# Kernel optimization log

Hardware: AMD Instinct MI355X
Metric: run time of the kernel (lower is better)

Reference implementation:

```python
import jax, jax.numpy as jnp
import numpy as np

H = 256  # hidden_dim
N = 500000  # num_orbitals
M = 8192  # num_molecules


def setup_inputs() -> dict:
    key = jax.random.key(0)
    ks = jax.random.split(key, 12)
    s = lambda fan_in: 1.0 / np.sqrt(fan_in)
    inp = {
        "orbital_embeddings": jax.random.normal(ks[0], (N, H), dtype=jnp.float32),
        "batch": jnp.sort(jax.random.randint(ks[1], (N,), 0, M, dtype=jnp.int32)),
        "num_molecules": M,
        # attention MLP: Linear(H, H//2) -> ReLU -> Linear(H//2, 1)
        "aW1": jax.random.uniform(ks[2], (H, H // 2), jnp.float32, -s(H), s(H)),
        "ab1": jnp.zeros((H // 2,), jnp.float32),
        "aW2": jax.random.uniform(ks[3], (H // 2, 1), jnp.float32, -s(H // 2), s(H // 2)),
        "ab2": jnp.zeros((1,), jnp.float32),
        # global head: Linear(H,H)->ReLU->Linear(H,H//2)->ReLU->Linear(H//2,1)
        "gW1": jax.random.uniform(ks[4], (H, H), jnp.float32, -s(H), s(H)),
        "gb1": jnp.zeros((H,), jnp.float32),
        "gW2": jax.random.uniform(ks[5], (H, H // 2), jnp.float32, -s(H), s(H)),
        "gb2": jnp.zeros((H // 2,), jnp.float32),
        "gW3": jax.random.uniform(ks[6], (H // 2, 1), jnp.float32, -s(H // 2), s(H // 2)),
        "gb3": jnp.zeros((1,), jnp.float32),
    }
    return inp


def reference(orbital_embeddings, batch, num_molecules, aW1, ab1, aW2, ab2,
              gW1, gb1, gW2, gb2, gW3, gb3):
    # attention logits: [N, 1] (dropout is identity in eval mode)
    h = jax.nn.relu(orbital_embeddings @ aW1 + ab1)
    logits = h @ aW2 + ab2  # [N, 1]

    # per-molecule (segment) softmax over orbitals, numerically stable
    lg = logits[:, 0]  # [N]
    seg_max = jax.ops.segment_max(lg, batch, num_segments=num_molecules)  # [M]
    seg_max = jnp.where(jnp.isfinite(seg_max), seg_max, 0.0)  # empty segments
    ex = jnp.exp(lg - seg_max[batch])  # [N]
    denom = jax.ops.segment_sum(ex, batch, num_segments=num_molecules)  # [M]
    w = ex / denom[batch]  # [N]

    # weighted scatter-add pooling -> [M, H]
    weighted = orbital_embeddings * w[:, None]
    mol = jax.ops.segment_sum(weighted, batch, num_segments=num_molecules)

    # global head MLP -> [M, 1]
    g = jax.nn.relu(mol @ gW1 + gb1)
    g = jax.nn.relu(g @ gW2 + gb2)
    return g @ gW3 + gb3
```

## Files before the change

kernel.cpp:

```cpp
#include <hip/hip_runtime.h>
#include <hip/hip_bf16.h>

#define H      256
#define CAP    64
#define GRID12 1024
#define MMAX   16

typedef _Float16 f16x8 __attribute__((ext_vector_type(8)));
typedef float    f32x4 __attribute__((ext_vector_type(4)));

__global__ __launch_bounds__(256) void k0_pack(
    const float* __restrict__ aW1, const float* __restrict__ gW1,
    const float* __restrict__ gW2,
    _Float16* __restrict__ aW1F, float* __restrict__ gW1P, float* __restrict__ gW2P)
{
    int idx = blockIdx.x * 256 + threadIdx.x;
    int stride = gridDim.x * 256;
    for (int e8 = idx; e8 < 4096; e8 += stride) {
        int l = e8 & 63, kknt = e8 >> 6;
        int kk = kknt & 7, nt = kknt >> 3;
        int j = nt*16 + (l & 15);
        int kbase = kk*32 + (l >> 4)*8;
        f16x8 v;
        #pragma unroll
        for (int e = 0; e < 8; ++e) v[e] = (_Float16)aW1[(kbase + e)*128 + j];
        *reinterpret_cast<f16x8*>(aW1F + e8*8) = v;
    }
    for (int e = idx; e < 64*256*4; e += stride) {
        int s = e & 3, j = (e >> 2) & 255, kq = e >> 10;
        gW1P[e] = gW1[(kq*4+s)*256 + j];
    }
    for (int e = idx; e < 64*128*4; e += stride) {
        int s = e & 3, j = (e >> 2) & 127, kq = e >> 9;
        gW2P[e] = gW2[(kq*4+s)*128 + j];
    }
}

__global__ __launch_bounds__(256) void k2a_starts(
    const int* __restrict__ batch, int* __restrict__ starts, int N, int M)
{
    int i = blockIdx.x * 256 + threadIdx.x;
    if (i >= N) return;
    int b = batch[i];
    if (i == 0) {
        for (int m = 0; m <= b; ++m) starts[m] = 0;
    } else {
        int p = batch[i-1];
        for (int m = p + 1; m <= b; ++m) starts[m] = i;
    }
    if (i == N - 1) {
        for (int m = b + 1; m <= M; ++m) starts[m] = N;
    }
}

__global__ __launch_bounds__(256) void k12_fused(
    const float* __restrict__ emb, const int* __restrict__ starts,
    const _Float16* __restrict__ aW1F, const float* __restrict__ ab1,
    const float* __restrict__ aW2, const float* __restrict__ ab2,
    float* __restrict__ mol, int M)
{
    __shared__ __align__(16) _Float16 eh[CAP * H];
    __shared__ float pr[4][CAP];
    __shared__ float wl[CAP];
    __shared__ int   sst[2*MMAX];

    const int t = threadIdx.x, w = t >> 6, l = t & 63;
    const int bid = blockIdx.x;
    char* ldsb = reinterpret_cast<char*>(eh);
    const f32x4 zero = {0.f, 0.f, 0.f, 0.f};

    if (t < 2*MMAX) {
        int idx = bid + (t >> 1)*GRID12 + (t & 1);
        sst[t] = starts[idx <= M ? idx : M];
    }

    f16x8 bf[2][8];
    #pragma unroll
    for (int nt2 = 0; nt2 < 2; ++nt2)
        #pragma unroll
        for (int kk = 0; kk < 8; ++kk)
            bf[nt2][kk] = *reinterpret_cast<const f16x8*>(
                aW1F + (size_t)(((2*w + nt2)*8 + kk)*64 + l)*8);

    float b1v[2], w2v[2];
    #pragma unroll
    for (int nt2 = 0; nt2 < 2; ++nt2) {
        int j = 32*w + nt2*16 + (l & 15);
        b1v[nt2] = ab1[j];
        w2v[nt2] = aW2[j];
    }
    const float bo = ab2[0];

    __syncthreads();

    int k = 0, start = 0, end = 0;
    for (;;) {
        if (k >= MMAX || bid + (size_t)k*GRID12 >= (size_t)M) return;
        start = sst[2*k]; end = sst[2*k+1];
        if (start < end) break;
        mol[(size_t)(bid + k*GRID12)*H + t] = 0.f;
        ++k;
    }

    int c0 = start;
    int cc = min(CAP, end - c0);
    float4 pv[16];

#define ISSUE(C0, CC) do {                                                      \
    _Pragma("unroll")                                                           \
    for (int j = 0; j < 8; ++j) {                                               \
        int ci = t + j*256;                                                     \
        int r = ci >> 5, c8 = ci & 31;                                          \
        int rr = r < (CC) ? r : (CC) - 1;                                       \
        const float4* pp = reinterpret_cast<const float4*>(                     \
            emb + (size_t)((C0) + rr)*H) + c8*2;                                \
        pv[2*j] = pp[0]; pv[2*j+1] = pp[1];                                     \
    } } while (0)

    ISSUE(c0, cc);
    float mx = -INFINITY, s = 0.f, acc = 0.f;

    for (;;) {
        const int  cur_m  = bid + k*GRID12;
        const int  cur_cc = cc;
        const bool last_chunk = (c0 + CAP >= end);

        __syncthreads();

        #pragma unroll
        for (int j = 0; j < 8; ++j) {
            int ci = t + j*256;
            int r = ci >> 5, c8 = ci & 31;
            float4 v0 = pv[2*j], v1 = pv[2*j+1];
            f16x8 hv;
            hv[0]=(_Float16)v0.x; hv[1]=(_Float16)v0.y; hv[2]=(_Float16)v0.z; hv[3]=(_Float16)v0.w;
            hv[4]=(_Float16)v1.x; hv[5]=(_Float16)v1.y; hv[6]=(_Float16)v1.z; hv[7]=(_Float16)v1.w;
            int wb = (r*512 + c8*16) ^ ((r & 7) << 4);
            *reinterpret_cast<f16x8*>(ldsb + wb) = hv;
        }

        int nk = k, nc0 = c0 + CAP, nend = end;
        bool have_next = true;
        if (last_chunk) {
            ++nk;
            for (;;) {
                if (nk >= MMAX || bid + (size_t)nk*GRID12 >= (size_t)M) { have_next = false; break; }
                int ns = sst[2*nk], ne = sst[2*nk+1];
                if (ns < ne) { nc0 = ns; nend = ne; break; }
                mol[(size_t)(bid + nk*GRID12)*H + t] = 0.f;
                ++nk;
            }
        }
        int ncc = 0;
        if (have_next) { ncc = min(CAP, nend - nc0); ISSUE(nc0, ncc); }
        __syncthreads();

        #pragma unroll
        for (int rt = 0; rt < 4; ++rt) {
            int row   = rt*16 + (l & 15);
            int rbase = row*512 + (l >> 4)*16;
            int swz   = (row & 7) << 4;
            f32x4 a20 = zero, a21 = zero;
            #pragma unroll
            for (int kk = 0; kk < 8; ++kk) {
                f16x8 af = *reinterpret_cast<const f16x8*>(ldsb + ((rbase + kk*64) ^ swz));
                a20 = __builtin_amdgcn_mfma_f32_16x16x32_f16(af, bf[0][kk], a20, 0, 0, 0);
                a21 = __builtin_amdgcn_mfma_f32_16x16x32_f16(af, bf[1][kk], a21, 0, 0, 0);
            }
            #pragma unroll
            for (int r = 0; r < 4; ++r) {
                float h0 = a20[r] + b1v[0]; h0 = h0 > 0.f ? h0 : 0.f;
                float h1 = a21[r] + b1v[1]; h1 = h1 > 0.f ? h1 : 0.f;
                float p = h0*w2v[0] + h1*w2v[1];
                p += __shfl_xor(p, 1, 64);
                p += __shfl_xor(p, 2, 64);
                p += __shfl_xor(p, 4, 64);
                p += __shfl_xor(p, 8, 64);
                if ((l & 15) == 0) pr[w][rt*16 + (l >> 4)*4 + r] = p;
            }
        }
        __syncthreads();

        float lg = -INFINITY;
        if (l < cur_cc) lg = pr[0][l] + pr[1][l] + pr[2][l] + pr[3][l] + bo;
        float mc = lg;
        mc = fmaxf(mc, __shfl_xor(mc, 1, 64));
        mc = fmaxf(mc, __shfl_xor(mc, 2, 64));
        mc = fmaxf(mc, __shfl_xor(mc, 4, 64));
        mc = fmaxf(mc, __shfl_xor(mc, 8, 64));
        mc = fmaxf(mc, __shfl_xor(mc, 16, 64));
        mc = fmaxf(mc, __shfl_xor(mc, 32, 64));
        float mxn = fmaxf(mx, mc);
        float rsc = __expf(mx - mxn);
        float e = (l < cur_cc) ? __expf(lg - mxn) : 0.f;
        float sc = e;
        sc += __shfl_xor(sc, 1, 64);
        sc += __shfl_xor(sc, 2, 64);
        sc += __shfl_xor(sc, 4, 64);
        sc += __shfl_xor(sc, 8, 64);
        sc += __shfl_xor(sc, 16, 64);
        sc += __shfl_xor(sc, 32, 64);
        s = s*rsc + sc;
        mx = mxn;
        if (w == 0) wl[l] = e;
        __syncthreads();

        acc *= rsc;
        #pragma unroll 16
        for (int g = 0; g < CAP; ++g) {
            _Float16 hv = *reinterpret_cast<const _Float16*>(
                ldsb + ((g*512 + t*2) ^ ((g & 7) << 4)));
            acc += wl[g] * (float)hv;
        }

        if (last_chunk) {
            mol[(size_t)cur_m*H + t] = acc / s;
            mx = -INFINITY; s = 0.f; acc = 0.f;
        }
        if (!have_next) return;
        k = nk; c0 = nc0; end = nend; cc = ncc;
    }
#undef ISSUE
}

__global__ __launch_bounds__(256) void k3_mlp(
    const float* __restrict__ mol, const float* __restrict__ gW1P,
    const float* __restrict__ gb1, const float* __restrict__ gW2P,
    const float* __restrict__ gb2, const float* __restrict__ gW3,
    const float* __restrict__ gb3, float* __restrict__ out, int M)
{
    __shared__ __align__(16) float mt[32 * 256];
    __shared__ __align__(16) float g1[32 * 256];
    __shared__ float tmp[4][16];
    int t = threadIdx.x;
    int blk = blockIdx.x;

    #pragma unroll
    for (int i = 0; i < 8; ++i) {
        int f = t + i*256;
        long gidx = (long)blk*2048 + f;
        float4 v = make_float4(0.f,0.f,0.f,0.f);
        if (gidx < (long)M*64) v = reinterpret_cast<const float4*>(mol)[gidx];
        reinterpret_cast<float4*>(mt)[f] = v;
    }
    __syncthreads();

    int j = t & 127, mh = t >> 7;

    float a0[16], a1[16];
    #pragma unroll
    for (int m = 0; m < 16; ++m) { a0[m] = 0.f; a1[m] = 0.f; }
    for (int kq = 0; kq < 64; ++kq) {
        float4 w0 = reinterpret_cast<const float4*>(gW1P)[kq*256 + j];
        float4 w1 = reinterpret_cast<const float4*>(gW1P)[kq*256 + j + 128];
        #pragma unroll
        for (int m = 0; m < 16; ++m) {
            float4 e = *reinterpret_cast<const float4*>(&mt[(mh*16 + m)*256 + kq*4]);
            a0[m] += e.x*w0.x + e.y*w0.y + e.z*w0.z + e.w*w0.w;
            a1[m] += e.x*w1.x + e.y*w1.y + e.z*w1.z + e.w*w1.w;
        }
    }
    {
        float b0 = gb1[j], b1 = gb1[j + 128];
        #pragma unroll
        for (int m = 0; m < 16; ++m) {
            float v0 = a0[m] + b0; v0 = v0 > 0.f ? v0 : 0.f;
            float v1 = a1[m] + b1; v1 = v1 > 0.f ? v1 : 0.f;
            g1[(mh*16 + m)*256 + j]       = v0;
            g1[(mh*16 + m)*256 + j + 128] = v1;
        }
    }
    __syncthreads();

    float a2[16];
    #pragma unroll
    for (int m = 0; m < 16; ++m) a2[m] = 0.f;
    for (int kq = 0; kq < 64; ++kq) {
        float4 w = reinterpret_cast<const float4*>(gW2P)[kq*128 + j];
        #pragma unroll
        for (int m = 0; m < 16; ++m) {
            float4 e = *reinterpret_cast<const float4*>(&g1[(mh*16 + m)*256 + kq*4]);
            a2[m] += e.x*w.x + e.y*w.y + e.z*w.z + e.w*w.w;
        }
    }

    float b2 = gb2[j], w3 = gW3[j];
    float p[16];
    #pragma unroll
    for (int m = 0; m < 16; ++m) {
        float v = a2[m] + b2; v = v > 0.f ? v : 0.f;
        p[m] = v * w3;
    }
    #pragma unroll
    for (int off = 32; off >= 1; off >>= 1) {
        #pragma unroll
        for (int m = 0; m < 16; ++m) p[m] += __shfl_xor(p[m], off, 64);
    }
    int wid = t >> 6;
    if ((t & 63) == 0) {
        #pragma unroll
        for (int m = 0; m < 16; ++m) tmp[wid][m] = p[m];
    }
    __syncthreads();
    if (t < 32) {
        int om = blk*32 + t;
        if (om < M) out[om] = tmp[(t >> 4)*2][t & 15] + tmp[(t >> 4)*2 + 1][t & 15] + gb3[0];
    }
}

extern "C" void kernel_launch(void* const* d_in, const int* in_sizes, int n_in,
                              void* d_out, int out_size, void* d_ws, size_t ws_size,
                              hipStream_t stream) {
    const float* emb  = (const float*)d_in[0];
    const int*   batch= (const int*)d_in[1];
    const float* aW1  = (const float*)d_in[3];
    const float* ab1  = (const float*)d_in[4];
    const float* aW2  = (const float*)d_in[5];
    const float* ab2  = (const float*)d_in[6];
    const float* gW1  = (const float*)d_in[7];
    const float* gb1  = (const float*)d_in[8];
    const float* gW2  = (const float*)d_in[9];
    const float* gb2  = (const float*)d_in[10];
    const float* gW3  = (const float*)d_in[11];
    const float* gb3  = (const float*)d_in[12];
    float* outp = (float*)d_out;

    int N = in_sizes[0] / H;
    int M = out_size;

    char* ws = (char*)d_ws;
    size_t off = 0;
    float*     mol    = (float*)(ws + off);    off += (8u<<20);
    _Float16*  aW1F   = (_Float16*)(ws + off); off += 65536;
    float*     gW1P   = (float*)(ws + off);    off += 262144;
    float*     gW2P   = (float*)(ws + off);    off += 131072;
    int*       starts = (int*)(ws + off);      off += (size_t)(M+1)*4;

    int g12 = M < GRID12 ? M : GRID12;

    k0_pack<<<64, 256, 0, stream>>>(aW1, gW1, gW2, aW1F, gW1P, gW2P);
    k2a_starts<<<(N + 255)/256, 256, 0, stream>>>(batch, starts, N, M);
    k12_fused<<<g12, 256, 0, stream>>>(emb, starts, aW1F, ab1, aW2, ab2, mol, M);
    k3_mlp<<<(M + 31)/32, 256, 0, stream>>>(mol, gW1P, gb1, gW2P, gb2, gW3, gb3, outp, M);
}
```

Before: 260.0 us.

## Use LDS-only barriers and double the fused kernel grid

Replaces __syncthreads in the fused attention/pooling kernel with barriers that wait only on LDS counters (lgkmcnt(0)), not on vmcnt. The prefetched global loads for the next chunk can then stay in flight across barriers. The grid also grows from 1024 to 2048 blocks, with the molecule stride passed at runtime, so each block handles fewer molecules and more blocks run at once. The risk is that the register-held prefetch is no longer drained at barriers, so correctness depends on the compiler inserting vmcnt waits before the prefetched values are used.

```diff
diff --git a/kernel.cpp b/kernel.cpp
--- a/kernel.cpp
+++ b/kernel.cpp
@@ -3,11 +3,16 @@
 
 #define H      256
 #define CAP    64
-#define GRID12 1024
+#define GRID12 2048
 #define MMAX   16
 
 typedef _Float16 f16x8 __attribute__((ext_vector_type(8)));
 typedef float    f32x4 __attribute__((ext_vector_type(4)));
+
+#define LGKM0()   asm volatile("s_waitcnt lgkmcnt(0)" ::: "memory")
+#define SBAR()    __builtin_amdgcn_s_barrier()
+#define SCHED0()  __builtin_amdgcn_sched_barrier(0)
+#define LDSBAR()  do { LGKM0(); SCHED0(); SBAR(); SCHED0(); } while (0)
 
 __global__ __launch_bounds__(256) void k0_pack(
     const float* __restrict__ aW1, const float* __restrict__ gW1,
@@ -57,7 +62,7 @@
     const float* __restrict__ emb, const int* __restrict__ starts,
     const _Float16* __restrict__ aW1F, const float* __restrict__ ab1,
     const float* __restrict__ aW2, const float* __restrict__ ab2,
-    float* __restrict__ mol, int M)
+    float* __restrict__ mol, int M, int gstride)
 {
     __shared__ __align__(16) _Float16 eh[CAP * H];
     __shared__ float pr[4][CAP];
@@ -70,7 +75,7 @@
     const f32x4 zero = {0.f, 0.f, 0.f, 0.f};
 
     if (t < 2*MMAX) {
-        int idx = bid + (t >> 1)*GRID12 + (t & 1);
+        long idx = (long)bid + (long)(t >> 1)*gstride + (t & 1);
         sst[t] = starts[idx <= M ? idx : M];
     }
 
@@ -95,10 +100,10 @@
 
     int k = 0, start = 0, end = 0;
     for (;;) {
-        if (k >= MMAX || bid + (size_t)k*GRID12 >= (size_t)M) return;
+        if (k >= MMAX || (long)bid + (long)k*gstride >= (long)M) return;
         start = sst[2*k]; end = sst[2*k+1];
         if (start < end) break;
-        mol[(size_t)(bid + k*GRID12)*H + t] = 0.f;
+        mol[((size_t)bid + (size_t)k*gstride)*H + t] = 0.f;
         ++k;
     }
 
@@ -121,11 +126,11 @@
     float mx = -INFINITY, s = 0.f, acc = 0.f;
 
     for (;;) {
-        const int  cur_m  = bid + k*GRID12;
-        const int  cur_cc = cc;
-        const bool last_chunk = (c0 + CAP >= end);
-
-        __syncthreads();
+        const size_t cur_m  = (size_t)bid + (size_t)k*gstride;
+        const int    cur_cc = cc;
+        const bool   last_chunk = (c0 + CAP >= end);
+
+        LDSBAR();
 
         #pragma unroll
         for (int j = 0; j < 8; ++j) {
@@ -144,16 +149,17 @@
         if (last_chunk) {
             ++nk;
             for (;;) {
-                if (nk >= MMAX || bid + (size_t)nk*GRID12 >= (size_t)M) { have_next = false; break; }
+                if (nk >= MMAX || (long)bid + (long)nk*gstride >= (long)M) { have_next = false; break; }
                 int ns = sst[2*nk], ne = sst[2*nk+1];
                 if (ns < ne) { nc0 = ns; nend = ne; break; }
-                mol[(size_t)(bid + nk*GRID12)*H + t] = 0.f;
+                mol[((size_t)bid + (size_t)nk*gstride)*H + t] = 0.f;
                 ++nk;
             }
         }
         int ncc = 0;
         if (have_next) { ncc = min(CAP, nend - nc0); ISSUE(nc0, ncc); }
-        __syncthreads();
+
+        LDSBAR();
 
         #pragma unroll
         for (int rt = 0; rt < 4; ++rt) {
@@ -179,7 +185,8 @@
                 if ((l & 15) == 0) pr[w][rt*16 + (l >> 4)*4 + r] = p;
             }
         }
-        __syncthreads();
+
+        LDSBAR();
 
         float lg = -INFINITY;
         if (l < cur_cc) lg = pr[0][l] + pr[1][l] + pr[2][l] + pr[3][l] + bo;
@@ -203,7 +210,8 @@
         s = s*rsc + sc;
         mx = mxn;
         if (w == 0) wl[l] = e;
-        __syncthreads();
+
+        LDSBAR();
 
         acc *= rsc;
         #pragma unroll 16
@@ -214,7 +222,7 @@
         }
 
         if (last_chunk) {
-            mol[(size_t)cur_m*H + t] = acc / s;
+            mol[cur_m*H + t] = acc / s;
             mx = -INFINITY; s = 0.f; acc = 0.f;
         }
         if (!have_next) return;
@@ -340,6 +348,6 @@
 
     k0_pack<<<64, 256, 0, stream>>>(aW1, gW1, gW2, aW1F, gW1P, gW2P);
     k2a_starts<<<(N + 255)/256, 256, 0, stream>>>(batch, starts, N, M);
-    k12_fused<<<g12, 256, 0, stream>>>(emb, starts, aW1F, ab1, aW2, ab2, mol, M);
+    k12_fused<<<g12, 256, 0, stream>>>(emb, starts, aW1F, ab1, aW2, ab2, mol, M, g12);
     k3_mlp<<<(M + 31)/32, 256, 0, stream>>>(mol, gW1P, gb1, gW2P, gb2, gW3, gb3, outp, M);
 }
```

New measurement: 268.8 us. 1.03x slower.
